# Kernel optimization log

Measured on AMD Instinct MI355X. Metric: run time of the kernel, lower is better.

Reference implementation:

```python
import jax, jax.numpy as jnp
import numpy as np

N_NODES = 100000


def gcn_conv(x, edge_src, edge_dst, edge_weight, W, b):
    # support = x @ W ; out = A @ support + b  (A given as weighted edge list)
    h = x @ W                                   # [N, d_out]
    msg = h[edge_src] * edge_weight[:, None]     # [E, d_out]
    agg = jax.ops.segment_sum(msg, edge_dst, num_segments=N_NODES)
    return agg + b


def setup_inputs() -> dict:
    key = jax.random.key(0)
    ks = jax.random.split(key, 8)
    N, E, m, hidden, m_y = N_NODES, 1600000, 128, 64, 32
    x = jax.random.normal(ks[0], (N, m), dtype=jnp.float32)
    edge_src = jax.random.randint(ks[1], (E,), 0, N, dtype=jnp.int32)
    edge_dst = jax.random.randint(ks[2], (E,), 0, N, dtype=jnp.int32)
    edge_weight = jax.random.uniform(ks[3], (E,), dtype=jnp.float32)
    s1 = 1.0 / np.sqrt(m)
    s2 = 1.0 / np.sqrt(hidden)
    W1 = jax.random.uniform(ks[4], (m, hidden), dtype=jnp.float32, minval=-s1, maxval=s1)
    b1 = jax.random.uniform(ks[5], (hidden,), dtype=jnp.float32, minval=-s1, maxval=s1)
    W2 = jax.random.uniform(ks[6], (hidden, m_y), dtype=jnp.float32, minval=-s2, maxval=s2)
    b2 = jax.random.uniform(ks[7], (m_y,), dtype=jnp.float32, minval=-s2, maxval=s2)
    return {"x": x, "edge_src": edge_src, "edge_dst": edge_dst,
            "edge_weight": edge_weight, "W1": W1, "b1": b1, "W2": W2, "b2": b2}


def reference(x, edge_src, edge_dst, edge_weight, W1, b1, W2, b2):
    out = gcn_conv(x, edge_src, edge_dst, edge_weight, W1, b1)
    out = jax.nn.relu(out)
    # F.dropout(p=0.5, training=self.training) -> identity in eval mode
    out = gcn_conv(out, edge_src, edge_dst, edge_weight, W2, b2)
    return out
```

## Files before the change

### kernel.cpp

```cpp
#include <hip/hip_runtime.h>
#include <hip/hip_bf16.h>


typedef unsigned short u16;
typedef unsigned int uint;
typedef short short8 __attribute__((ext_vector_type(8)));
typedef float floatx4 __attribute__((ext_vector_type(4)));

static __device__ __forceinline__ u16 f2bf(float f) {
    unsigned int u = __float_as_uint(f);
    return (u16)((u + 0x7fff + ((u >> 16) & 1)) >> 16);
}

#define F4C(v, j) ((j)==0?(v).x:((j)==1?(v).y:((j)==2?(v).z:(v).w)))
#define CHUNK 4096
#define ECAP 384

union SharedU {
    struct {
        u16 xs[64][136];
        u16 wf[4][4][64][8];
    } g;
    struct {
        int2 stage[CHUNK];
        u16  stb[CHUNK];
        int  hist[512], sc[512], xscan[512], place[512], runbase[512];
    } p;
};

__global__ __launch_bounds__(256, 3) void g1p_kernel(
    const float* __restrict__ x, const float* __restrict__ W1,
    u16* __restrict__ h1, int N,
    const int* __restrict__ src, const int* __restrict__ dst,
    const float* __restrict__ w, int* __restrict__ gcursor,
    int2* __restrict__ es, int E, int cap, int pblocks)
{
    __shared__ SharedU sh;
    const int tid = threadIdx.x;

    if (blockIdx.x < pblocks) {
        const int base = blockIdx.x * CHUNK;
        const int nloc = min(CHUNK, E - base);

        sh.p.hist[tid] = 0; sh.p.hist[tid + 256] = 0;
        __syncthreads();
        for (int i = tid; i < nloc; i += 256)
            atomicAdd(&sh.p.hist[dst[base + i] >> 8], 1);
        __syncthreads();

        sh.p.sc[tid] = sh.p.hist[tid];
        sh.p.sc[tid + 256] = sh.p.hist[tid + 256];
        __syncthreads();
        for (int o = 1; o < 512; o <<= 1) {
            int v0 = (tid >= o) ? sh.p.sc[tid - o] : 0;
            int v1 = (tid + 256 >= o) ? sh.p.sc[tid + 256 - o] : 0;
            __syncthreads();
            sh.p.sc[tid] += v0;
            sh.p.sc[tid + 256] += v1;
            __syncthreads();
        }
        sh.p.xscan[tid] = sh.p.sc[tid] - sh.p.hist[tid];
        sh.p.xscan[tid + 256] = sh.p.sc[tid + 256] - sh.p.hist[tid + 256];
        sh.p.place[tid] = sh.p.xscan[tid];
        sh.p.place[tid + 256] = sh.p.xscan[tid + 256];
        __syncthreads();

        for (int i = tid; i < nloc; i += 256) {
            int d = dst[base + i];
            int b = d >> 8;
            int pos = atomicAdd(&sh.p.place[b], 1);
            sh.p.stage[pos] = make_int2(src[base + i] | ((d & 255) << 24),
                                        __float_as_int(w[base + i]));
            sh.p.stb[pos] = (u16)b;
        }
        __syncthreads();

        {
            int l0 = sh.p.hist[tid], l1 = sh.p.hist[tid + 256];
            sh.p.runbase[tid]       = l0 ? atomicAdd(&gcursor[tid], l0)       : 0;
            sh.p.runbase[tid + 256] = l1 ? atomicAdd(&gcursor[tid + 256], l1) : 0;
        }
        __syncthreads();

        for (int i = tid; i < nloc; i += 256) {
            int b = sh.p.stb[i];
            es[(size_t)b * cap + sh.p.runbase[b] + (i - sh.p.xscan[b])] = sh.p.stage[i];
        }
        return;
    }

    const int row0 = (blockIdx.x - pblocks) * 64;
    {
        const float4* W4 = (const float4*)W1;
        #pragma unroll
        for (int i = 0; i < 8; i++) {
            int idx = tid + i*256;
            int k = idx >> 4, n4 = (idx & 15) * 4;
            float4 v = W4[idx];
            int step = k >> 5, klane = (k >> 3) & 3, j = k & 7;
            #pragma unroll
            for (int c = 0; c < 4; c++) {
                int n = n4 + c;
                sh.g.wf[n >> 4][step][klane*16 + (n & 15)][j] = f2bf(F4C(v, c));
            }
        }
    }
    {
        const float4* x4 = (const float4*)x;
        #pragma unroll
        for (int i = 0; i < 8; i++) {
            int idx = tid + i*256;
            int r = idx >> 5, kc = idx & 31;
            int gr = row0 + r;
            float4 v = make_float4(0.f,0.f,0.f,0.f);
            if (gr < N) v = x4[gr*32 + kc];
            ushort4 o;
            o.x = f2bf(v.x); o.y = f2bf(v.y); o.z = f2bf(v.z); o.w = f2bf(v.w);
            *(ushort4*)&sh.g.xs[r][kc*4] = o;
        }
    }
    __syncthreads();

    const int wave = tid >> 6, lane = tid & 63;
    const int m = lane & 15, quad = lane >> 4;
    const int rw = wave * 16;

    floatx4 acc[4] = {(floatx4)(0.f), (floatx4)(0.f), (floatx4)(0.f), (floatx4)(0.f)};
    #pragma unroll
    for (int step = 0; step < 4; step++) {
        short8 a = *(const short8*)&sh.g.xs[rw + m][step*32 + quad*8];
        #pragma unroll
        for (int nt = 0; nt < 4; nt++) {
            short8 b = *(const short8*)&sh.g.wf[nt][step][lane][0];
            acc[nt] = __builtin_amdgcn_mfma_f32_16x16x32_bf16(a, b, acc[nt], 0, 0, 0);
        }
    }
    #pragma unroll
    for (int nt = 0; nt < 4; nt++) {
        #pragma unroll
        for (int r = 0; r < 4; r++) {
            int gr = row0 + rw + quad*4 + r;
            if (gr < N) h1[(size_t)gr*64 + nt*16 + m] = f2bf(acc[nt][r]);
        }
    }
}

#define SCAP 6144
__global__ __launch_bounds__(512, 3) void sort2_kernel(
    const int2* __restrict__ es, const int* __restrict__ gcursor,
    int2* __restrict__ es2, int2* __restrict__ off2, int N, int cap, int nb)
{
    __shared__ int2 stage[SCAP];
    __shared__ int hist[256], sc[256], cur[256];
    const int t = threadIdx.x;
    const int b = blockIdx.x;
    const int e0 = b * cap;
    const int len = gcursor[b];
    const int nstage = min(len, SCAP);

    if (t < 256) hist[t] = 0;
    __syncthreads();
    for (int i = t; i < nstage; i += 512) {
        int2 e = es[e0 + i];
        stage[i] = e;
        atomicAdd(&hist[((unsigned)e.x) >> 24], 1);
    }
    for (int i = SCAP + t; i < len; i += 512)
        atomicAdd(&hist[((unsigned)es[e0 + i].x) >> 24], 1);
    __syncthreads();

    int v = 0;
    if (t < 256) { v = hist[t]; sc[t] = v; }
    __syncthreads();
    for (int o = 1; o < 256; o <<= 1) {
        int add = 0;
        if (t < 256 && t >= o) add = sc[t - o];
        __syncthreads();
        if (t < 256) sc[t] += add;
        __syncthreads();
    }
    if (t < 256) {
        int ex = sc[t] - v;
        cur[t] = ex;
        int g = b * 256 + t;
        if (g < N) off2[g] = make_int2(e0 + ex, e0 + ex + v);
    }
    __syncthreads();

    for (int i = t; i < nstage; i += 512) {
        int2 e = stage[i];
        int pos = e0 + atomicAdd(&cur[((unsigned)e.x) >> 24], 1);
        es2[pos] = e;
    }
    for (int i = SCAP + t; i < len; i += 512) {
        int2 e = es[e0 + i];
        int pos = e0 + atomicAdd(&cur[((unsigned)e.x) >> 24], 1);
        es2[pos] = e;
    }
}

__global__ __launch_bounds__(256, 6) void gather1_kernel(
    const u16* __restrict__ h1, const int2* __restrict__ es,
    const int2* __restrict__ off2, const float* __restrict__ b1,
    const float* __restrict__ W2, u16* __restrict__ h2, int N)
{
    __shared__ __align__(16) u16 ts[64][72];
    __shared__ __align__(16) u16 wf2[2][2][64][8];
    __shared__ float b1s[64];
    __shared__ int2 eb[4][ECAP];
    const int tid = threadIdx.x;

    {
        const float4* s4 = (const float4*)W2;
        #pragma unroll
        for (int i = 0; i < 2; i++) {
            int idx = tid + i*256;
            float4 v = s4[idx];
            int k = idx >> 3, n4 = (idx & 7) * 4;
            int step = k >> 5, quad = (k >> 3) & 3, j = k & 7;
            #pragma unroll
            for (int c = 0; c < 4; c++) {
                int n = n4 + c;
                wf2[n >> 4][step][quad*16 + (n & 15)][j] = f2bf(F4C(v, c));
            }
        }
        if (tid < 16) ((float4*)b1s)[tid] = ((const float4*)b1)[tid];
    }
    __syncthreads();

    const int wave = tid >> 6, lane = tid & 63;
    const int h = lane >> 4, fl = lane & 15;
    const int node0 = blockIdx.x * 64 + wave * 16;
    const uint2* h1v = (const uint2*)h1;
    uint* tsu = (uint*)&ts[0][0];

    const int2 sg = off2[min(node0 + fl, N - 1)];
    const int beg = __builtin_amdgcn_readfirstlane(sg.x);
    const int end = __builtin_amdgcn_readlane(sg.y, 15);
    const int len = end - beg;

    if (len <= ECAP) {
        for (int k = lane; k < len; k += 64) eb[wave][k] = es[beg + k];

        #pragma unroll 1
        for (int i = 0; i < 16; i++) {
            const int pbeg = __builtin_amdgcn_readlane(sg.x, i) - beg;
            const int pend = __builtin_amdgcn_readlane(sg.y, i) - beg;
            const int cl = pend - 1;
            float a0 = 0.f, a1 = 0.f, a2 = 0.f, a3 = 0.f;
            #pragma unroll 1
            for (int p = pbeg; p < pend; p += 16) {
                const int i0 = p + h, i1 = p + 4 + h, i2 = p + 8 + h, i3 = p + 12 + h;
                int2 e0 = eb[wave][min(i0, cl)];
                int2 e1 = eb[wave][min(i1, cl)];
                int2 e2 = eb[wave][min(i2, cl)];
                int2 e3 = eb[wave][min(i3, cl)];
                uint2 v0 = h1v[(size_t)(e0.x & 0xFFFFFF) * 16 + fl];
                uint2 v1 = h1v[(size_t)(e1.x & 0xFFFFFF) * 16 + fl];
                uint2 v2 = h1v[(size_t)(e2.x & 0xFFFFFF) * 16 + fl];
                uint2 v3 = h1v[(size_t)(e3.x & 0xFFFFFF) * 16 + fl];
                float w0 = (i0 < pend) ? __int_as_float(e0.y) : 0.f;
                float w1 = (i1 < pend) ? __int_as_float(e1.y) : 0.f;
                float w2 = (i2 < pend) ? __int_as_float(e2.y) : 0.f;
                float w3 = (i3 < pend) ? __int_as_float(e3.y) : 0.f;
                a0 += __uint_as_float(v0.x << 16) * w0 + __uint_as_float(v1.x << 16) * w1
                    + __uint_as_float(v2.x << 16) * w2 + __uint_as_float(v3.x << 16) * w3;
                a1 += __uint_as_float(v0.x & 0xFFFF0000u) * w0 + __uint_as_float(v1.x & 0xFFFF0000u) * w1
                    + __uint_as_float(v2.x & 0xFFFF0000u) * w2 + __uint_as_float(v3.x & 0xFFFF0000u) * w3;
                a2 += __uint_as_float(v0.y << 16) * w0 + __uint_as_float(v1.y << 16) * w1
                    + __uint_as_float(v2.y << 16) * w2 + __uint_as_float(v3.y << 16) * w3;
                a3 += __uint_as_float(v0.y & 0xFFFF0000u) * w0 + __uint_as_float(v1.y & 0xFFFF0000u) * w1
                    + __uint_as_float(v2.y & 0xFFFF0000u) * w2 + __uint_as_float(v3.y & 0xFFFF0000u) * w3;
            }
            a0 += __shfl_xor(a0, 16, 64); a1 += __shfl_xor(a1, 16, 64);
            a2 += __shfl_xor(a2, 16, 64); a3 += __shfl_xor(a3, 16, 64);
            a0 += __shfl_xor(a0, 32, 64); a1 += __shfl_xor(a1, 32, 64);
            a2 += __shfl_xor(a2, 32, 64); a3 += __shfl_xor(a3, 32, 64);
            if (h == 0) {
                uint t0 = (uint)f2bf(fmaxf(a0 + b1s[4*fl],     0.f))
                        | ((uint)f2bf(fmaxf(a1 + b1s[4*fl + 1], 0.f)) << 16);
                uint t1 = (uint)f2bf(fmaxf(a2 + b1s[4*fl + 2], 0.f))
                        | ((uint)f2bf(fmaxf(a3 + b1s[4*fl + 3], 0.f)) << 16);
                *(uint2*)&tsu[(wave*16 + i) * 36 + 2*fl] = make_uint2(t0, t1);
            }
        }
    } else {
        #pragma unroll 1
        for (int i = 0; i < 16; i++) {
            const int pbeg = __builtin_amdgcn_readlane(sg.x, i);
            const int pend = __builtin_amdgcn_readlane(sg.y, i);
            const int cl = pend - 1;
            float a0 = 0.f, a1 = 0.f, a2 = 0.f, a3 = 0.f;
            #pragma unroll 1
            for (int p = pbeg; p < pend; p += 16) {
                const int i0 = p + h, i1 = p + 4 + h, i2 = p + 8 + h, i3 = p + 12 + h;
                int2 e0 = es[min(i0, cl)];
                int2 e1 = es[min(i1, cl)];
                int2 e2 = es[min(i2, cl)];
                int2 e3 = es[min(i3, cl)];
                uint2 v0 = h1v[(size_t)(e0.x & 0xFFFFFF) * 16 + fl];
                uint2 v1 = h1v[(size_t)(e1.x & 0xFFFFFF) * 16 + fl];
                uint2 v2 = h1v[(size_t)(e2.x & 0xFFFFFF) * 16 + fl];
                uint2 v3 = h1v[(size_t)(e3.x & 0xFFFFFF) * 16 + fl];
                float w0 = (i0 < pend) ? __int_as_float(e0.y) : 0.f;
                float w1 = (i1 < pend) ? __int_as_float(e1.y) : 0.f;
                float w2 = (i2 < pend) ? __int_as_float(e2.y) : 0.f;
                float w3 = (i3 < pend) ? __int_as_float(e3.y) : 0.f;
                a0 += __uint_as_float(v0.x << 16) * w0 + __uint_as_float(v1.x << 16) * w1
                    + __uint_as_float(v2.x << 16) * w2 + __uint_as_float(v3.x << 16) * w3;
                a1 += __uint_as_float(v0.x & 0xFFFF0000u) * w0 + __uint_as_float(v1.x & 0xFFFF0000u) * w1
                    + __uint_as_float(v2.x & 0xFFFF0000u) * w2 + __uint_as_float(v3.x & 0xFFFF0000u) * w3;
                a2 += __uint_as_float(v0.y << 16) * w0 + __uint_as_float(v1.y << 16) * w1
                    + __uint_as_float(v2.y << 16) * w2 + __uint_as_float(v3.y << 16) * w3;
                a3 += __uint_as_float(v0.y & 0xFFFF0000u) * w0 + __uint_as_float(v1.y & 0xFFFF0000u) * w1
                    + __uint_as_float(v2.y & 0xFFFF0000u) * w2 + __uint_as_float(v3.y & 0xFFFF0000u) * w3;
            }
            a0 += __shfl_xor(a0, 16, 64); a1 += __shfl_xor(a1, 16, 64);
            a2 += __shfl_xor(a2, 16, 64); a3 += __shfl_xor(a3, 16, 64);
            a0 += __shfl_xor(a0, 32, 64); a1 += __shfl_xor(a1, 32, 64);
            a2 += __shfl_xor(a2, 32, 64); a3 += __shfl_xor(a3, 32, 64);
            if (h == 0) {
                uint t0 = (uint)f2bf(fmaxf(a0 + b1s[4*fl],     0.f))
                        | ((uint)f2bf(fmaxf(a1 + b1s[4*fl + 1], 0.f)) << 16);
                uint t1 = (uint)f2bf(fmaxf(a2 + b1s[4*fl + 2], 0.f))
                        | ((uint)f2bf(fmaxf(a3 + b1s[4*fl + 3], 0.f)) << 16);
                *(uint2*)&tsu[(wave*16 + i) * 36 + 2*fl] = make_uint2(t0, t1);
            }
        }
    }

    const int m = lane & 15, quad = lane >> 4;
    floatx4 acc[2] = {(floatx4)(0.f), (floatx4)(0.f)};
    #pragma unroll
    for (int step = 0; step < 2; step++) {
        short8 a = *(const short8*)&ts[wave*16 + m][step*32 + quad*8];
        #pragma unroll
        for (int nt = 0; nt < 2; nt++) {
            short8 b = *(const short8*)&wf2[nt][step][lane][0];
            acc[nt] = __builtin_amdgcn_mfma_f32_16x16x32_bf16(a, b, acc[nt], 0, 0, 0);
        }
    }
    #pragma unroll
    for (int nt = 0; nt < 2; nt++) {
        #pragma unroll
        for (int r = 0; r < 4; r++) {
            int g = node0 + quad*4 + r;
            if (g < N) h2[(size_t)g*32 + nt*16 + m] = f2bf(acc[nt][r]);
        }
    }
}

__global__ __launch_bounds__(256) void gather2_kernel(
    const u16* __restrict__ h2, const int2* __restrict__ es,
    const int2* __restrict__ off2, const float* __restrict__ b2,
    float* __restrict__ out, int N)
{
    __shared__ int2 eb[4][ECAP];
    const int tid = threadIdx.x;
    const int wave = tid >> 6, lane = tid & 63;
    const int g = lane >> 3, fl = lane & 7;
    const int node0 = blockIdx.x * 64 + wave * 16;
    const uint2* h2v = (const uint2*)h2;

    const int2 sg = off2[min(node0 + (lane & 15), N - 1)];
    const int beg = __builtin_amdgcn_readfirstlane(sg.x);
    const int end = __builtin_amdgcn_readlane(sg.y, 15);
    const int len = end - beg;
    const float4 bb = ((const float4*)b2)[fl];

    if (len <= ECAP) {
        for (int k = lane; k < len; k += 64) eb[wave][k] = es[beg + k];

        #pragma unroll 1
        for (int i = 0; i < 16; i++) {
            const int pbeg = __builtin_amdgcn_readlane(sg.x, i) - beg;
            const int pend = __builtin_amdgcn_readlane(sg.y, i) - beg;
            const int cl = pend - 1;
            float a0 = 0.f, a1 = 0.f, a2 = 0.f, a3 = 0.f;
            #pragma unroll 1
            for (int p = pbeg; p < pend; p += 32) {
                const int i0 = p + g, i1 = p + 8 + g, i2 = p + 16 + g, i3 = p + 24 + g;
                int2 e0 = eb[wave][min(i0, cl)];
                int2 e1 = eb[wave][min(i1, cl)];
                int2 e2 = eb[wave][min(i2, cl)];
                int2 e3 = eb[wave][min(i3, cl)];
                uint2 v0 = h2v[(size_t)(e0.x & 0xFFFFFF) * 8 + fl];
                uint2 v1 = h2v[(size_t)(e1.x & 0xFFFFFF) * 8 + fl];
                uint2 v2 = h2v[(size_t)(e2.x & 0xFFFFFF) * 8 + fl];
                uint2 v3 = h2v[(size_t)(e3.x & 0xFFFFFF) * 8 + fl];
                float w0 = (i0 < pend) ? __int_as_float(e0.y) : 0.f;
                float w1 = (i1 < pend) ? __int_as_float(e1.y) : 0.f;
                float w2 = (i2 < pend) ? __int_as_float(e2.y) : 0.f;
                float w3 = (i3 < pend) ? __int_as_float(e3.y) : 0.f;
                a0 += __uint_as_float(v0.x << 16) * w0 + __uint_as_float(v1.x << 16) * w1
                    + __uint_as_float(v2.x << 16) * w2 + __uint_as_float(v3.x << 16) * w3;
                a1 += __uint_as_float(v0.x & 0xFFFF0000u) * w0 + __uint_as_float(v1.x & 0xFFFF0000u) * w1
                    + __uint_as_float(v2.x & 0xFFFF0000u) * w2 + __uint_as_float(v3.x & 0xFFFF0000u) * w3;
                a2 += __uint_as_float(v0.y << 16) * w0 + __uint_as_float(v1.y << 16) * w1
                    + __uint_as_float(v2.y << 16) * w2 + __uint_as_float(v3.y << 16) * w3;
                a3 += __uint_as_float(v0.y & 0xFFFF0000u) * w0 + __uint_as_float(v1.y & 0xFFFF0000u) * w1
                    + __uint_as_float(v2.y & 0xFFFF0000u) * w2 + __uint_as_float(v3.y & 0xFFFF0000u) * w3;
            }
            a0 += __shfl_xor(a0, 8, 64);  a1 += __shfl_xor(a1, 8, 64);
            a2 += __shfl_xor(a2, 8, 64);  a3 += __shfl_xor(a3, 8, 64);
            a0 += __shfl_xor(a0, 16, 64); a1 += __shfl_xor(a1, 16, 64);
            a2 += __shfl_xor(a2, 16, 64); a3 += __shfl_xor(a3, 16, 64);
            a0 += __shfl_xor(a0, 32, 64); a1 += __shfl_xor(a1, 32, 64);
            a2 += __shfl_xor(a2, 32, 64); a3 += __shfl_xor(a3, 32, 64);
            const int d = node0 + i;
            if (g == 0 && d < N)
                *(float4*)&out[(size_t)d * 32 + 4 * fl] =
                    make_float4(a0 + bb.x, a1 + bb.y, a2 + bb.z, a3 + bb.w);
        }
    } else {
        #pragma unroll 1
        for (int i = 0; i < 16; i++) {
            const int pbeg = __builtin_amdgcn_readlane(sg.x, i);
            const int pend = __builtin_amdgcn_readlane(sg.y, i);
            const int cl = pend - 1;
            float a0 = 0.f, a1 = 0.f, a2 = 0.f, a3 = 0.f;
            #pragma unroll 1
            for (int p = pbeg; p < pend; p += 32) {
                const int i0 = p + g, i1 = p + 8 + g, i2 = p + 16 + g, i3 = p + 24 + g;
                int2 e0 = es[min(i0, cl)];
                int2 e1 = es[min(i1, cl)];
                int2 e2 = es[min(i2, cl)];
                int2 e3 = es[min(i3, cl)];
                uint2 v0 = h2v[(size_t)(e0.x & 0xFFFFFF) * 8 + fl];
                uint2 v1 = h2v[(size_t)(e1.x & 0xFFFFFF) * 8 + fl];
                uint2 v2 = h2v[(size_t)(e2.x & 0xFFFFFF) * 8 + fl];
                uint2 v3 = h2v[(size_t)(e3.x & 0xFFFFFF) * 8 + fl];
                float w0 = (i0 < pend) ? __int_as_float(e0.y) : 0.f;
                float w1 = (i1 < pend) ? __int_as_float(e1.y) : 0.f;
                float w2 = (i2 < pend) ? __int_as_float(e2.y) : 0.f;
                float w3 = (i3 < pend) ? __int_as_float(e3.y) : 0.f;
                a0 += __uint_as_float(v0.x << 16) * w0 + __uint_as_float(v1.x << 16) * w1
                    + __uint_as_float(v2.x << 16) * w2 + __uint_as_float(v3.x << 16) * w3;
                a1 += __uint_as_float(v0.x & 0xFFFF0000u) * w0 + __uint_as_float(v1.x & 0xFFFF0000u) * w1
                    + __uint_as_float(v2.x & 0xFFFF0000u) * w2 + __uint_as_float(v3.x & 0xFFFF0000u) * w3;
                a2 += __uint_as_float(v0.y << 16) * w0 + __uint_as_float(v1.y << 16) * w1
                    + __uint_as_float(v2.y << 16) * w2 + __uint_as_float(v3.y << 16) * w3;
                a3 += __uint_as_float(v0.y & 0xFFFF0000u) * w0 + __uint_as_float(v1.y & 0xFFFF0000u) * w1
                    + __uint_as_float(v2.y & 0xFFFF0000u) * w2 + __uint_as_float(v3.y & 0xFFFF0000u) * w3;
            }
            a0 += __shfl_xor(a0, 8, 64);  a1 += __shfl_xor(a1, 8, 64);
            a2 += __shfl_xor(a2, 8, 64);  a3 += __shfl_xor(a3, 8, 64);
            a0 += __shfl_xor(a0, 16, 64); a1 += __shfl_xor(a1, 16, 64);
            a2 += __shfl_xor(a2, 16, 64); a3 += __shfl_xor(a3, 16, 64);
            a0 += __shfl_xor(a0, 32, 64); a1 += __shfl_xor(a1, 32, 64);
            a2 += __shfl_xor(a2, 32, 64); a3 += __shfl_xor(a3, 32, 64);
            const int d = node0 + i;
            if (g == 0 && d < N)
                *(float4*)&out[(size_t)d * 32 + 4 * fl] =
                    make_float4(a0 + bb.x, a1 + bb.y, a2 + bb.z, a3 + bb.w);
        }
    }
}

extern "C" void kernel_launch(void* const* d_in, const int* in_sizes, int n_in,
                              void* d_out, int out_size, void* d_ws, size_t ws_size,
                              hipStream_t stream)
{
    const float* x   = (const float*)d_in[0];
    const int*  esrc = (const int*)d_in[1];
    const int*  edst = (const int*)d_in[2];
    const float* ew  = (const float*)d_in[3];
    const float* W1  = (const float*)d_in[4];
    const float* b1  = (const float*)d_in[5];
    const float* W2  = (const float*)d_in[6];
    const float* b2  = (const float*)d_in[7];
    float* out = (float*)d_out;

    const int N = in_sizes[0] / 128;
    const int E = in_sizes[1];
    const int nb = (N + 255) >> 8;

    const int mean = (E + nb - 1) / nb;
    int s = 1; while (s * s < mean) s++;
    const int cap = (mean + 8 * s + 15) & ~15;

    char* base = (char*)d_ws;
    size_t o = 0;
    auto alloc = [&](size_t bytes) { char* p = base + o; o = (o + bytes + 255) & ~(size_t)255; return p; };
    u16*  h1      = (u16*) alloc((size_t)N * 64 * 2);
    u16*  h2      = (u16*) alloc((size_t)N * 32 * 2);
    int2* es      = (int2*)alloc((size_t)nb * cap * 8);
    int2* es2     = (int2*)alloc((size_t)nb * cap * 8);
    int2* off2    = (int2*)alloc((size_t)N * 8);
    int*  gcursor = (int*) alloc(512 * 4);

    const int pblocks = (E + CHUNK - 1) / CHUNK;
    const int gblocks = (N + 63) / 64;

    hipMemsetAsync(gcursor, 0, 512 * 4, stream);
    g1p_kernel<<<pblocks + gblocks, 256, 0, stream>>>(
        x, W1, h1, N, esrc, edst, ew, gcursor, es, E, cap, pblocks);
    sort2_kernel<<<nb, 512, 0, stream>>>(es, gcursor, es2, off2, N, cap, nb);
    gather1_kernel<<<(N + 63) / 64, 256, 0, stream>>>(h1, es2, off2, b1, W2, h2, N);
    gather2_kernel<<<(N + 63) / 64, 256, 0, stream>>>(h2, es2, off2, b2, out, N);
}
```

Baseline: 214.4 us.

## Pre-pack W1 once, drop LDS edge staging, raise occupancy bounds

A small init kernel now converts W1 to bf16 in its MFMA fragment layout and zeroes the bucket cursors, replacing the memset and the per-block W1 conversion in g1p. The partition chunk is halved so more blocks share the edge-bucketing work. Both gather kernels drop the LDS edge-staging buffer and read edges directly from global memory, and their launch bounds are raised to allow more resident waves. The trade is losing LDS reuse of edge records in exchange for higher occupancy, plus one extra tiny kernel launch.

```diff
diff --git a/kernel.cpp b/kernel.cpp
--- a/kernel.cpp
+++ b/kernel.cpp
@@ -13,10 +13,24 @@
 }
 
 #define F4C(v, j) ((j)==0?(v).x:((j)==1?(v).y:((j)==2?(v).z:(v).w)))
-#define CHUNK 4096
-#define ECAP 384
-
-union SharedU {
+#define CHUNK 2048
+
+__global__ __launch_bounds__(256) void init_kernel(
+    const float* __restrict__ W1, u16* __restrict__ wfg, int* __restrict__ gcursor)
+{
+    const int idx = blockIdx.x * 256 + threadIdx.x;
+    if (idx < 512) gcursor[idx] = 0;
+    const float4 v = ((const float4*)W1)[idx];
+    const int k = idx >> 4, n4 = (idx & 15) * 4;
+    const int step = k >> 5, klane = (k >> 3) & 3, j = k & 7;
+    #pragma unroll
+    for (int c = 0; c < 4; c++) {
+        int n = n4 + c;
+        wfg[(((n >> 4) * 4 + step) * 64 + klane * 16 + (n & 15)) * 8 + j] = f2bf(F4C(v, c));
+    }
+}
+
+union __align__(16) SharedU {
     struct {
         u16 xs[64][136];
         u16 wf[4][4][64][8];
@@ -28,8 +42,8 @@
     } p;
 };
 
-__global__ __launch_bounds__(256, 3) void g1p_kernel(
-    const float* __restrict__ x, const float* __restrict__ W1,
+__global__ __launch_bounds__(256, 4) void g1p_kernel(
+    const float* __restrict__ x, const u16* __restrict__ wfg,
     u16* __restrict__ h1, int N,
     const int* __restrict__ src, const int* __restrict__ dst,
     const float* __restrict__ w, int* __restrict__ gcursor,
@@ -91,19 +105,10 @@
 
     const int row0 = (blockIdx.x - pblocks) * 64;
     {
-        const float4* W4 = (const float4*)W1;
-        #pragma unroll
-        for (int i = 0; i < 8; i++) {
-            int idx = tid + i*256;
-            int k = idx >> 4, n4 = (idx & 15) * 4;
-            float4 v = W4[idx];
-            int step = k >> 5, klane = (k >> 3) & 3, j = k & 7;
-            #pragma unroll
-            for (int c = 0; c < 4; c++) {
-                int n = n4 + c;
-                sh.g.wf[n >> 4][step][klane*16 + (n & 15)][j] = f2bf(F4C(v, c));
-            }
-        }
+        const float4* wg4 = (const float4*)wfg;
+        float4* wl4 = (float4*)&sh.g.wf[0][0][0][0];
+        #pragma unroll
+        for (int i = 0; i < 4; i++) wl4[tid + i*256] = wg4[tid + i*256];
     }
     {
         const float4* x4 = (const float4*)x;
@@ -199,7 +204,7 @@
     }
 }
 
-__global__ __launch_bounds__(256, 6) void gather1_kernel(
+__global__ __launch_bounds__(256, 8) void gather1_kernel(
     const u16* __restrict__ h1, const int2* __restrict__ es,
     const int2* __restrict__ off2, const float* __restrict__ b1,
     const float* __restrict__ W2, u16* __restrict__ h2, int N)
@@ -207,7 +212,6 @@
     __shared__ __align__(16) u16 ts[64][72];
     __shared__ __align__(16) u16 wf2[2][2][64][8];
     __shared__ float b1s[64];
-    __shared__ int2 eb[4][ECAP];
     const int tid = threadIdx.x;
 
     {
@@ -235,97 +239,47 @@
     uint* tsu = (uint*)&ts[0][0];
 
     const int2 sg = off2[min(node0 + fl, N - 1)];
-    const int beg = __builtin_amdgcn_readfirstlane(sg.x);
-    const int end = __builtin_amdgcn_readlane(sg.y, 15);
-    const int len = end - beg;
-
-    if (len <= ECAP) {
-        for (int k = lane; k < len; k += 64) eb[wave][k] = es[beg + k];
-
+
+    #pragma unroll 1
+    for (int i = 0; i < 16; i++) {
+        const int pbeg = __builtin_amdgcn_readlane(sg.x, i);
+        const int pend = __builtin_amdgcn_readlane(sg.y, i);
+        const int cl = pend - 1;
+        float a0 = 0.f, a1 = 0.f, a2 = 0.f, a3 = 0.f;
         #pragma unroll 1
-        for (int i = 0; i < 16; i++) {
-            const int pbeg = __builtin_amdgcn_readlane(sg.x, i) - beg;
-            const int pend = __builtin_amdgcn_readlane(sg.y, i) - beg;
-            const int cl = pend - 1;
-            float a0 = 0.f, a1 = 0.f, a2 = 0.f, a3 = 0.f;
-            #pragma unroll 1
-            for (int p = pbeg; p < pend; p += 16) {
-                const int i0 = p + h, i1 = p + 4 + h, i2 = p + 8 + h, i3 = p + 12 + h;
-                int2 e0 = eb[wave][min(i0, cl)];
-                int2 e1 = eb[wave][min(i1, cl)];
-                int2 e2 = eb[wave][min(i2, cl)];
-                int2 e3 = eb[wave][min(i3, cl)];
-                uint2 v0 = h1v[(size_t)(e0.x & 0xFFFFFF) * 16 + fl];
-                uint2 v1 = h1v[(size_t)(e1.x & 0xFFFFFF) * 16 + fl];
-                uint2 v2 = h1v[(size_t)(e2.x & 0xFFFFFF) * 16 + fl];
-                uint2 v3 = h1v[(size_t)(e3.x & 0xFFFFFF) * 16 + fl];
-                float w0 = (i0 < pend) ? __int_as_float(e0.y) : 0.f;
-                float w1 = (i1 < pend) ? __int_as_float(e1.y) : 0.f;
-                float w2 = (i2 < pend) ? __int_as_float(e2.y) : 0.f;
-                float w3 = (i3 < pend) ? __int_as_float(e3.y) : 0.f;
-                a0 += __uint_as_float(v0.x << 16) * w0 + __uint_as_float(v1.x << 16) * w1
-                    + __uint_as_float(v2.x << 16) * w2 + __uint_as_float(v3.x << 16) * w3;
-                a1 += __uint_as_float(v0.x & 0xFFFF0000u) * w0 + __uint_as_float(v1.x & 0xFFFF0000u) * w1
-                    + __uint_as_float(v2.x & 0xFFFF0000u) * w2 + __uint_as_float(v3.x & 0xFFFF0000u) * w3;
-                a2 += __uint_as_float(v0.y << 16) * w0 + __uint_as_float(v1.y << 16) * w1
-                    + __uint_as_float(v2.y << 16) * w2 + __uint_as_float(v3.y << 16) * w3;
-                a3 += __uint_as_float(v0.y & 0xFFFF0000u) * w0 + __uint_as_float(v1.y & 0xFFFF0000u) * w1
-                    + __uint_as_float(v2.y & 0xFFFF0000u) * w2 + __uint_as_float(v3.y & 0xFFFF0000u) * w3;
-            }
-            a0 += __shfl_xor(a0, 16, 64); a1 += __shfl_xor(a1, 16, 64);
-            a2 += __shfl_xor(a2, 16, 64); a3 += __shfl_xor(a3, 16, 64);
-            a0 += __shfl_xor(a0, 32, 64); a1 += __shfl_xor(a1, 32, 64);
-            a2 += __shfl_xor(a2, 32, 64); a3 += __shfl_xor(a3, 32, 64);
-            if (h == 0) {
-                uint t0 = (uint)f2bf(fmaxf(a0 + b1s[4*fl],     0.f))
-                        | ((uint)f2bf(fmaxf(a1 + b1s[4*fl + 1], 0.f)) << 16);
-                uint t1 = (uint)f2bf(fmaxf(a2 + b1s[4*fl + 2], 0.f))
-                        | ((uint)f2bf(fmaxf(a3 + b1s[4*fl + 3], 0.f)) << 16);
-                *(uint2*)&tsu[(wave*16 + i) * 36 + 2*fl] = make_uint2(t0, t1);
-            }
-        }
-    } else {
-        #pragma unroll 1
-        for (int i = 0; i < 16; i++) {
-            const int pbeg = __builtin_amdgcn_readlane(sg.x, i);
-            const int pend = __builtin_amdgcn_readlane(sg.y, i);
-            const int cl = pend - 1;
-            float a0 = 0.f, a1 = 0.f, a2 = 0.f, a3 = 0.f;
-            #pragma unroll 1
-            for (int p = pbeg; p < pend; p += 16) {
-                const int i0 = p + h, i1 = p + 4 + h, i2 = p + 8 + h, i3 = p + 12 + h;
-                int2 e0 = es[min(i0, cl)];
-                int2 e1 = es[min(i1, cl)];
-                int2 e2 = es[min(i2, cl)];
-                int2 e3 = es[min(i3, cl)];
-                uint2 v0 = h1v[(size_t)(e0.x & 0xFFFFFF) * 16 + fl];
-                uint2 v1 = h1v[(size_t)(e1.x & 0xFFFFFF) * 16 + fl];
-                uint2 v2 = h1v[(size_t)(e2.x & 0xFFFFFF) * 16 + fl];
-                uint2 v3 = h1v[(size_t)(e3.x & 0xFFFFFF) * 16 + fl];
-                float w0 = (i0 < pend) ? __int_as_float(e0.y) : 0.f;
-                float w1 = (i1 < pend) ? __int_as_float(e1.y) : 0.f;
-                float w2 = (i2 < pend) ? __int_as_float(e2.y) : 0.f;
-                float w3 = (i3 < pend) ? __int_as_float(e3.y) : 0.f;
-                a0 += __uint_as_float(v0.x << 16) * w0 + __uint_as_float(v1.x << 16) * w1
-                    + __uint_as_float(v2.x << 16) * w2 + __uint_as_float(v3.x << 16) * w3;
-                a1 += __uint_as_float(v0.x & 0xFFFF0000u) * w0 + __uint_as_float(v1.x & 0xFFFF0000u) * w1
-                    + __uint_as_float(v2.x & 0xFFFF0000u) * w2 + __uint_as_float(v3.x & 0xFFFF0000u) * w3;
-                a2 += __uint_as_float(v0.y << 16) * w0 + __uint_as_float(v1.y << 16) * w1
-                    + __uint_as_float(v2.y << 16) * w2 + __uint_as_float(v3.y << 16) * w3;
-                a3 += __uint_as_float(v0.y & 0xFFFF0000u) * w0 + __uint_as_float(v1.y & 0xFFFF0000u) * w1
-                    + __uint_as_float(v2.y & 0xFFFF0000u) * w2 + __uint_as_float(v3.y & 0xFFFF0000u) * w3;
-            }
-            a0 += __shfl_xor(a0, 16, 64); a1 += __shfl_xor(a1, 16, 64);
-            a2 += __shfl_xor(a2, 16, 64); a3 += __shfl_xor(a3, 16, 64);
-            a0 += __shfl_xor(a0, 32, 64); a1 += __shfl_xor(a1, 32, 64);
-            a2 += __shfl_xor(a2, 32, 64); a3 += __shfl_xor(a3, 32, 64);
-            if (h == 0) {
-                uint t0 = (uint)f2bf(fmaxf(a0 + b1s[4*fl],     0.f))
-                        | ((uint)f2bf(fmaxf(a1 + b1s[4*fl + 1], 0.f)) << 16);
-                uint t1 = (uint)f2bf(fmaxf(a2 + b1s[4*fl + 2], 0.f))
-                        | ((uint)f2bf(fmaxf(a3 + b1s[4*fl + 3], 0.f)) << 16);
-                *(uint2*)&tsu[(wave*16 + i) * 36 + 2*fl] = make_uint2(t0, t1);
-            }
+        for (int p = pbeg; p < pend; p += 16) {
+            const int i0 = p + h, i1 = p + 4 + h, i2 = p + 8 + h, i3 = p + 12 + h;
+            int2 e0 = es[min(i0, cl)];
+            int2 e1 = es[min(i1, cl)];
+            int2 e2 = es[min(i2, cl)];
+            int2 e3 = es[min(i3, cl)];
+            uint2 v0 = h1v[(size_t)(e0.x & 0xFFFFFF) * 16 + fl];
+            uint2 v1 = h1v[(size_t)(e1.x & 0xFFFFFF) * 16 + fl];
+            uint2 v2 = h1v[(size_t)(e2.x & 0xFFFFFF) * 16 + fl];
+            uint2 v3 = h1v[(size_t)(e3.x & 0xFFFFFF) * 16 + fl];
+            float w0 = (i0 < pend) ? __int_as_float(e0.y) : 0.f;
+            float w1 = (i1 < pend) ? __int_as_float(e1.y) : 0.f;
+            float w2 = (i2 < pend) ? __int_as_float(e2.y) : 0.f;
+            float w3 = (i3 < pend) ? __int_as_float(e3.y) : 0.f;
+            a0 += __uint_as_float(v0.x << 16) * w0 + __uint_as_float(v1.x << 16) * w1
+                + __uint_as_float(v2.x << 16) * w2 + __uint_as_float(v3.x << 16) * w3;
+            a1 += __uint_as_float(v0.x & 0xFFFF0000u) * w0 + __uint_as_float(v1.x & 0xFFFF0000u) * w1
+                + __uint_as_float(v2.x & 0xFFFF0000u) * w2 + __uint_as_float(v3.x & 0xFFFF0000u) * w3;
+            a2 += __uint_as_float(v0.y << 16) * w0 + __uint_as_float(v1.y << 16) * w1
+                + __uint_as_float(v2.y << 16) * w2 + __uint_as_float(v3.y << 16) * w3;
+            a3 += __uint_as_float(v0.y & 0xFFFF0000u) * w0 + __uint_as_float(v1.y & 0xFFFF0000u) * w1
+                + __uint_as_float(v2.y & 0xFFFF0000u) * w2 + __uint_as_float(v3.y & 0xFFFF0000u) * w3;
+        }
+        a0 += __shfl_xor(a0, 16, 64); a1 += __shfl_xor(a1, 16, 64);
+        a2 += __shfl_xor(a2, 16, 64); a3 += __shfl_xor(a3, 16, 64);
+        a0 += __shfl_xor(a0, 32, 64); a1 += __shfl_xor(a1, 32, 64);
+        a2 += __shfl_xor(a2, 32, 64); a3 += __shfl_xor(a3, 32, 64);
+        if (h == 0) {
+            uint t0 = (uint)f2bf(fmaxf(a0 + b1s[4*fl],     0.f))
+                    | ((uint)f2bf(fmaxf(a1 + b1s[4*fl + 1], 0.f)) << 16);
+            uint t1 = (uint)f2bf(fmaxf(a2 + b1s[4*fl + 2], 0.f))
+                    | ((uint)f2bf(fmaxf(a3 + b1s[4*fl + 3], 0.f)) << 16);
+            *(uint2*)&tsu[(wave*16 + i) * 36 + 2*fl] = make_uint2(t0, t1);
         }
     }
 
@@ -350,12 +304,11 @@
     }
 }
 
-__global__ __launch_bounds__(256) void gather2_kernel(
+__global__ __launch_bounds__(256, 8) void gather2_kernel(
     const u16* __restrict__ h2, const int2* __restrict__ es,
     const int2* __restrict__ off2, const float* __restrict__ b2,
     float* __restrict__ out, int N)
 {
-    __shared__ int2 eb[4][ECAP];
     const int tid = threadIdx.x;
     const int wave = tid >> 6, lane = tid & 63;
     const int g = lane >> 3, fl = lane & 7;
@@ -363,97 +316,48 @@
     const uint2* h2v = (const uint2*)h2;
 
     const int2 sg = off2[min(node0 + (lane & 15), N - 1)];
-    const int beg = __builtin_amdgcn_readfirstlane(sg.x);
-    const int end = __builtin_amdgcn_readlane(sg.y, 15);
-    const int len = end - beg;
     const float4 bb = ((const float4*)b2)[fl];
 
-    if (len <= ECAP) {
-        for (int k = lane; k < len; k += 64) eb[wave][k] = es[beg + k];
-
+    #pragma unroll 1
+    for (int i = 0; i < 16; i++) {
+        const int pbeg = __builtin_amdgcn_readlane(sg.x, i);
+        const int pend = __builtin_amdgcn_readlane(sg.y, i);
+        const int cl = pend - 1;
+        float a0 = 0.f, a1 = 0.f, a2 = 0.f, a3 = 0.f;
         #pragma unroll 1
-        for (int i = 0; i < 16; i++) {
-            const int pbeg = __builtin_amdgcn_readlane(sg.x, i) - beg;
-            const int pend = __builtin_amdgcn_readlane(sg.y, i) - beg;
-            const int cl = pend - 1;
-            float a0 = 0.f, a1 = 0.f, a2 = 0.f, a3 = 0.f;
-            #pragma unroll 1
-            for (int p = pbeg; p < pend; p += 32) {
-                const int i0 = p + g, i1 = p + 8 + g, i2 = p + 16 + g, i3 = p + 24 + g;
-                int2 e0 = eb[wave][min(i0, cl)];
-                int2 e1 = eb[wave][min(i1, cl)];
-                int2 e2 = eb[wave][min(i2, cl)];
-                int2 e3 = eb[wave][min(i3, cl)];
-                uint2 v0 = h2v[(size_t)(e0.x & 0xFFFFFF) * 8 + fl];
-                uint2 v1 = h2v[(size_t)(e1.x & 0xFFFFFF) * 8 + fl];
-                uint2 v2 = h2v[(size_t)(e2.x & 0xFFFFFF) * 8 + fl];
-                uint2 v3 = h2v[(size_t)(e3.x & 0xFFFFFF) * 8 + fl];
-                float w0 = (i0 < pend) ? __int_as_float(e0.y) : 0.f;
-                float w1 = (i1 < pend) ? __int_as_float(e1.y) : 0.f;
-                float w2 = (i2 < pend) ? __int_as_float(e2.y) : 0.f;
-                float w3 = (i3 < pend) ? __int_as_float(e3.y) : 0.f;
-                a0 += __uint_as_float(v0.x << 16) * w0 + __uint_as_float(v1.x << 16) * w1
-                    + __uint_as_float(v2.x << 16) * w2 + __uint_as_float(v3.x << 16) * w3;
-                a1 += __uint_as_float(v0.x & 0xFFFF0000u) * w0 + __uint_as_float(v1.x & 0xFFFF0000u) * w1
-                    + __uint_as_float(v2.x & 0xFFFF0000u) * w2 + __uint_as_float(v3.x & 0xFFFF0000u) * w3;
-                a2 += __uint_as_float(v0.y << 16) * w0 + __uint_as_float(v1.y << 16) * w1
-                    + __uint_as_float(v2.y << 16) * w2 + __uint_as_float(v3.y << 16) * w3;
-                a3 += __uint_as_float(v0.y & 0xFFFF0000u) * w0 + __uint_as_float(v1.y & 0xFFFF0000u) * w1
-                    + __uint_as_float(v2.y & 0xFFFF0000u) * w2 + __uint_as_float(v3.y & 0xFFFF0000u) * w3;
-            }
-            a0 += __shfl_xor(a0, 8, 64);  a1 += __shfl_xor(a1, 8, 64);
-            a2 += __shfl_xor(a2, 8, 64);  a3 += __shfl_xor(a3, 8, 64);
-            a0 += __shfl_xor(a0, 16, 64); a1 += __shfl_xor(a1, 16, 64);
-            a2 += __shfl_xor(a2, 16, 64); a3 += __shfl_xor(a3, 16, 64);
-            a0 += __shfl_xor(a0, 32, 64); a1 += __shfl_xor(a1, 32, 64);
-            a2 += __shfl_xor(a2, 32, 64); a3 += __shfl_xor(a3, 32, 64);
-            const int d = node0 + i;
-            if (g == 0 && d < N)
-                *(float4*)&out[(size_t)d * 32 + 4 * fl] =
-                    make_float4(a0 + bb.x, a1 + bb.y, a2 + bb.z, a3 + bb.w);
-        }
-    } else {
-        #pragma unroll 1
-        for (int i = 0; i < 16; i++) {
-            const int pbeg = __builtin_amdgcn_readlane(sg.x, i);
-            const int pend = __builtin_amdgcn_readlane(sg.y, i);
-            const int cl = pend - 1;
-            float a0 = 0.f, a1 = 0.f, a2 = 0.f, a3 = 0.f;
-            #pragma unroll 1
-            for (int p = pbeg; p < pend; p += 32) {
-                const int i0 = p + g, i1 = p + 8 + g, i2 = p + 16 + g, i3 = p + 24 + g;
-                int2 e0 = es[min(i0, cl)];
-                int2 e1 = es[min(i1, cl)];
-                int2 e2 = es[min(i2, cl)];
-                int2 e3 = es[min(i3, cl)];
-                uint2 v0 = h2v[(size_t)(e0.x & 0xFFFFFF) * 8 + fl];
-                uint2 v1 = h2v[(size_t)(e1.x & 0xFFFFFF) * 8 + fl];
-                uint2 v2 = h2v[(size_t)(e2.x & 0xFFFFFF) * 8 + fl];
-                uint2 v3 = h2v[(size_t)(e3.x & 0xFFFFFF) * 8 + fl];
-                float w0 = (i0 < pend) ? __int_as_float(e0.y) : 0.f;
-                float w1 = (i1 < pend) ? __int_as_float(e1.y) : 0.f;
-                float w2 = (i2 < pend) ? __int_as_float(e2.y) : 0.f;
-                float w3 = (i3 < pend) ? __int_as_float(e3.y) : 0.f;
-                a0 += __uint_as_float(v0.x << 16) * w0 + __uint_as_float(v1.x << 16) * w1
-                    + __uint_as_float(v2.x << 16) * w2 + __uint_as_float(v3.x << 16) * w3;
-                a1 += __uint_as_float(v0.x & 0xFFFF0000u) * w0 + __uint_as_float(v1.x & 0xFFFF0000u) * w1
-                    + __uint_as_float(v2.x & 0xFFFF0000u) * w2 + __uint_as_float(v3.x & 0xFFFF0000u) * w3;
-                a2 += __uint_as_float(v0.y << 16) * w0 + __uint_as_float(v1.y << 16) * w1
-                    + __uint_as_float(v2.y << 16) * w2 + __uint_as_float(v3.y << 16) * w3;
-                a3 += __uint_as_float(v0.y & 0xFFFF0000u) * w0 + __uint_as_float(v1.y & 0xFFFF0000u) * w1
-                    + __uint_as_float(v2.y & 0xFFFF0000u) * w2 + __uint_as_float(v3.y & 0xFFFF0000u) * w3;
-            }
-            a0 += __shfl_xor(a0, 8, 64);  a1 += __shfl_xor(a1, 8, 64);
-            a2 += __shfl_xor(a2, 8, 64);  a3 += __shfl_xor(a3, 8, 64);
-            a0 += __shfl_xor(a0, 16, 64); a1 += __shfl_xor(a1, 16, 64);
-            a2 += __shfl_xor(a2, 16, 64); a3 += __shfl_xor(a3, 16, 64);
-            a0 += __shfl_xor(a0, 32, 64); a1 += __shfl_xor(a1, 32, 64);
-            a2 += __shfl_xor(a2, 32, 64); a3 += __shfl_xor(a3, 32, 64);
-            const int d = node0 + i;
-            if (g == 0 && d < N)
-                *(float4*)&out[(size_t)d * 32 + 4 * fl] =
-                    make_float4(a0 + bb.x, a1 + bb.y, a2 + bb.z, a3 + bb.w);
-        }
+        for (int p = pbeg; p < pend; p += 32) {
+            const int i0 = p + g, i1 = p + 8 + g, i2 = p + 16 + g, i3 = p + 24 + g;
+            int2 e0 = es[min(i0, cl)];
+            int2 e1 = es[min(i1, cl)];
+            int2 e2 = es[min(i2, cl)];
+            int2 e3 = es[min(i3, cl)];
+            uint2 v0 = h2v[(size_t)(e0.x & 0xFFFFFF) * 8 + fl];
+            uint2 v1 = h2v[(size_t)(e1.x & 0xFFFFFF) * 8 + fl];
+            uint2 v2 = h2v[(size_t)(e2.x & 0xFFFFFF) * 8 + fl];
+            uint2 v3 = h2v[(size_t)(e3.x & 0xFFFFFF) * 8 + fl];
+            float w0 = (i0 < pend) ? __int_as_float(e0.y) : 0.f;
+            float w1 = (i1 < pend) ? __int_as_float(e1.y) : 0.f;
+            float w2 = (i2 < pend) ? __int_as_float(e2.y) : 0.f;
+            float w3 = (i3 < pend) ? __int_as_float(e3.y) : 0.f;
+            a0 += __uint_as_float(v0.x << 16) * w0 + __uint_as_float(v1.x << 16) * w1
+                + __uint_as_float(v2.x << 16) * w2 + __uint_as_float(v3.x << 16) * w3;
+            a1 += __uint_as_float(v0.x & 0xFFFF0000u) * w0 + __uint_as_float(v1.x & 0xFFFF0000u) * w1
+                + __uint_as_float(v2.x & 0xFFFF0000u) * w2 + __uint_as_float(v3.x & 0xFFFF0000u) * w3;
+            a2 += __uint_as_float(v0.y << 16) * w0 + __uint_as_float(v1.y << 16) * w1
+                + __uint_as_float(v2.y << 16) * w2 + __uint_as_float(v3.y << 16) * w3;
+            a3 += __uint_as_float(v0.y & 0xFFFF0000u) * w0 + __uint_as_float(v1.y & 0xFFFF0000u) * w1
+                + __uint_as_float(v2.y & 0xFFFF0000u) * w2 + __uint_as_float(v3.y & 0xFFFF0000u) * w3;
+        }
+        a0 += __shfl_xor(a0, 8, 64);  a1 += __shfl_xor(a1, 8, 64);
+        a2 += __shfl_xor(a2, 8, 64);  a3 += __shfl_xor(a3, 8, 64);
+        a0 += __shfl_xor(a0, 16, 64); a1 += __shfl_xor(a1, 16, 64);
+        a2 += __shfl_xor(a2, 16, 64); a3 += __shfl_xor(a3, 16, 64);
+        a0 += __shfl_xor(a0, 32, 64); a1 += __shfl_xor(a1, 32, 64);
+        a2 += __shfl_xor(a2, 32, 64); a3 += __shfl_xor(a3, 32, 64);
+        const int d = node0 + i;
+        if (g == 0 && d < N)
+            *(float4*)&out[(size_t)d * 32 + 4 * fl] =
+                make_float4(a0 + bb.x, a1 + bb.y, a2 + bb.z, a3 + bb.w);
     }
 }
 
@@ -488,13 +392,14 @@
     int2* es2     = (int2*)alloc((size_t)nb * cap * 8);
     int2* off2    = (int2*)alloc((size_t)N * 8);
     int*  gcursor = (int*) alloc(512 * 4);
+    u16*  wfg     = (u16*) alloc(8192 * 2);
 
     const int pblocks = (E + CHUNK - 1) / CHUNK;
     const int gblocks = (N + 63) / 64;
 
-    hipMemsetAsync(gcursor, 0, 512 * 4, stream);
+    init_kernel<<<8, 256, 0, stream>>>(W1, wfg, gcursor);
     g1p_kernel<<<pblocks + gblocks, 256, 0, stream>>>(
-        x, W1, h1, N, esrc, edst, ew, gcursor, es, E, cap, pblocks);
+        x, wfg, h1, N, esrc, edst, ew, gcursor, es, E, cap, pblocks);
     sort2_kernel<<<nb, 512, 0, stream>>>(es, gcursor, es2, off2, N, cap, nb);
     gather1_kernel<<<(N + 63) / 64, 256, 0, stream>>>(h1, es2, off2, b1, W2, h2, N);
     gather2_kernel<<<(N + 63) / 64, 256, 0, stream>>>(h2, es2, off2, b2, out, N);
```

After: 237.7 us. 1.11x slower.
